# Kernel tuning notes

Measured on AMD Instinct MI355X. Metric: run time of the kernel, lower is better.

The kernel has to match this reference:

```python
import jax, jax.numpy as jnp
import numpy as np

N = 50000   # nodes
E = 1600000 # edges
G = 256     # graphs
EPS = 1e-5  # batchnorm eps (torch default)


def _bn(h, g, b):
    # training-mode BatchNorm1d: biased batch stats
    m = h.mean(0)
    v = h.var(0)
    return (h - m) * jax.lax.rsqrt(v + EPS) * g + b


def _mlp(h, W1, b1, g, be, W2, b2):
    # Lin -> BN -> ReLU -> Lin
    h = jax.nn.relu(_bn(h @ W1 + b1, g, be))
    return h @ W2 + b2


def _scatter_mean(v, idx, n):
    s = jax.ops.segment_sum(v, idx, num_segments=n)
    c = jax.ops.segment_sum(jnp.ones((v.shape[0], 1), v.dtype), idx, num_segments=n)
    return s / jnp.maximum(c, 1.0)


def setup_inputs() -> dict:
    key = jax.random.key(0)
    ks = iter(jax.random.split(key, 32))
    d = {}
    d["x"] = jax.random.normal(next(ks), (N, 48), dtype=jnp.float32)
    d["edge_index"] = jax.random.randint(next(ks), (2, E), 0, N, dtype=jnp.int64)
    d["batch"] = jnp.sort(jax.random.randint(next(ks), (N,), 0, G, dtype=jnp.int64))

    def lin(k, fin, fout):
        kw, kb = jax.random.split(k)
        s = 1.0 / np.sqrt(fin)
        return (jax.random.uniform(kw, (fin, fout), jnp.float32, -s, s),
                jax.random.uniform(kb, (fout,), jnp.float32, -s, s))

    # input BatchNorm1d(48)
    d["bn_g"] = jnp.ones((48,), jnp.float32)
    d["bn_b"] = jnp.zeros((48,), jnp.float32)

    def mlp_params(prefix, fin, fmid, fout):
        W1, b1 = lin(next(ks), fin, fmid)
        W2, b2 = lin(next(ks), fmid, fout)
        d[prefix + "_W1"], d[prefix + "_b1"] = W1, b1
        d[prefix + "_g"] = jnp.ones((fmid,), jnp.float32)
        d[prefix + "_be"] = jnp.zeros((fmid,), jnp.float32)
        d[prefix + "_W2"], d[prefix + "_b2"] = W2, b2

    mlp_params("e", 96, 128, 128)    # EdgeBlock
    mlp_params("n1", 176, 128, 128)  # NodeBlock mlp1
    mlp_params("n2", 176, 128, 128)  # NodeBlock mlp2
    mlp_params("gl", 128, 128, 2)    # GlobalBlock
    return d


def reference(x, edge_index, batch, bn_g, bn_b,
              e_W1, e_b1, e_g, e_be, e_W2, e_b2,
              n1_W1, n1_b1, n1_g, n1_be, n1_W2, n1_b2,
              n2_W1, n2_b1, n2_g, n2_be, n2_W2, n2_b2,
              gl_W1, gl_b1, gl_g, gl_be, gl_W2, gl_b2):
    x = _bn(x, bn_g, bn_b)
    row, col = edge_index[0], edge_index[1]
    # EdgeBlock: cat(src, dest) -> MLP
    edge_attr = _mlp(jnp.concatenate([x[row], x[col]], axis=1),
                     e_W1, e_b1, e_g, e_be, e_W2, e_b2)
    # NodeBlock: cat(x[row], edge_attr) -> mlp1 -> scatter_mean(col) -> cat(x,.) -> mlp2
    m = _mlp(jnp.concatenate([x[row], edge_attr], axis=1),
             n1_W1, n1_b1, n1_g, n1_be, n1_W2, n1_b2)
    agg = _scatter_mean(m, col, N)
    x2 = _mlp(jnp.concatenate([x, agg], axis=1),
              n2_W1, n2_b1, n2_g, n2_be, n2_W2, n2_b2)
    # GlobalBlock: scatter_mean over graphs -> MLP -> [G, 2]
    u = _scatter_mean(x2, batch, G)
    u = _mlp(u, gl_W1, gl_b1, gl_g, gl_be, gl_W2, gl_b2)
    return u
```

## Files before the change

### kernel.cpp

```cpp
#include <hip/hip_runtime.h>
#include <hip/hip_bf16.h>
#include <stdint.h>

#define DEV static __device__ __forceinline__

constexpr int N_ = 50000;
constexpr int E_ = 1600000;
constexpr int G_ = 256;

typedef __attribute__((ext_vector_type(8))) short short8;
typedef __attribute__((ext_vector_type(4))) float float4v;

DEV uint16_t f2bf(float f){
  uint32_t u = __float_as_uint(f);
  uint32_t r = (u + 0x7fffu + ((u >> 16) & 1u)) >> 16;
  return (uint16_t)r;
}
DEV float bf2f(uint16_t v){ return __uint_as_float((uint32_t)v << 16); }
DEV void unpack2(uint32_t p, float& a, float& b){
  a = __uint_as_float(p << 16);
  b = __uint_as_float(p & 0xffff0000u);
}
DEV uint32_t pack2(float a, float b){
  return (uint32_t)f2bf(a) | ((uint32_t)f2bf(b) << 16);
}
DEV short8 lds_load8(const uint16_t* p){
  union { short8 v; uint2 u[2]; } c;
  c.u[0] = *(const uint2*)p;
  c.u[1] = *(const uint2*)(p + 4);
  return c.v;
}
DEV void lds_store16B_as8(uint32_t* d, uint4 v){
  *(uint2*)d       = make_uint2(v.x, v.y);
  *(uint2*)(d + 2) = make_uint2(v.z, v.w);
}

__global__ __launch_bounds__(256) void k_xstats(const float* __restrict__ x, float* __restrict__ xstats){
  __shared__ float lst[96];
  int t = threadIdx.x;
  if (t < 96) lst[t] = 0.f;
  __syncthreads();
  int gid = blockIdx.x * 256 + t;
  int c4 = (gid % 12) * 4;
  float s[4] = {0,0,0,0}, q[4] = {0,0,0,0};
  const float4v* x4 = (const float4v*)x;
  for (int i = gid; i < N_ * 12; i += 64512){
    float4v v = x4[i];
    #pragma unroll
    for (int j = 0; j < 4; j++){ s[j] += v[j]; q[j] += v[j]*v[j]; }
  }
  #pragma unroll
  for (int j = 0; j < 4; j++){
    atomicAdd(&lst[c4 + j], s[j]);
    atomicAdd(&lst[48 + c4 + j], q[j]);
  }
  __syncthreads();
  if (t < 96) atomicAdd(&xstats[t], lst[t]);
}

__global__ void k_xfin(const float* __restrict__ xstats, const float* __restrict__ g,
                       const float* __restrict__ b, float* __restrict__ sx, float* __restrict__ tx){
  int c = threadIdx.x;
  if (c < 48){
    float m = xstats[c] / (float)N_;
    float v = xstats[48 + c] / (float)N_ - m*m;
    float s = g[c] / sqrtf(v + 1e-5f);
    sx[c] = s; tx[c] = b[c] - m*s;
  }
}

__global__ __launch_bounds__(256) void k_hist(const int* __restrict__ ei, int* __restrict__ counts){
  int e = blockIdx.x * 256 + threadIdx.x;
  if (e < E_) atomicAdd(&counts[ei[E_ + e]], 1);
}

__global__ __launch_bounds__(256) void k_invc(const int* __restrict__ counts, float* __restrict__ invc){
  int n = blockIdx.x * 256 + threadIdx.x;
  if (n < N_){ int c = counts[n]; invc[n] = (c > 0) ? 1.f/(float)c : 0.f; }
}

__global__ __launch_bounds__(256) void k_scan(const int* __restrict__ counts, int* __restrict__ off, int* __restrict__ cur){
  __shared__ int wsum[4];
  __shared__ int carry_s;
  int t = threadIdx.x, lane = t & 63, w = t >> 6;
  if (t == 0) carry_s = 0;
  __syncthreads();
  for (int base = 0; base < N_; base += 1024){
    int i0 = base + t * 4;
    int v0 = (i0 + 0 < N_) ? counts[i0 + 0] : 0;
    int v1 = (i0 + 1 < N_) ? counts[i0 + 1] : 0;
    int v2 = (i0 + 2 < N_) ? counts[i0 + 2] : 0;
    int v3 = (i0 + 3 < N_) ? counts[i0 + 3] : 0;
    int tsum = v0 + v1 + v2 + v3;
    int xs = tsum;
    for (int d = 1; d < 64; d <<= 1){ int y = __shfl_up(xs, d); if (lane >= d) xs += y; }
    if (lane == 63) wsum[w] = xs;
    __syncthreads();
    int woff = 0;
    for (int k = 0; k < w; k++) woff += wsum[k];
    int excl = xs - tsum + woff + carry_s;
    int e0 = excl, e1 = e0 + v0, e2 = e1 + v1, e3 = e2 + v2;
    if (i0 + 0 < N_){ off[i0+0] = e0; cur[i0+0] = e0; }
    if (i0 + 1 < N_){ off[i0+1] = e1; cur[i0+1] = e1; }
    if (i0 + 2 < N_){ off[i0+2] = e2; cur[i0+2] = e2; }
    if (i0 + 3 < N_){ off[i0+3] = e3; cur[i0+3] = e3; }
    __syncthreads();
    if (t == 0) carry_s += wsum[0] + wsum[1] + wsum[2] + wsum[3];
    __syncthreads();
  }
  if (t == 0) off[N_] = carry_s;
}

__global__ __launch_bounds__(256) void k_place(const int* __restrict__ ei, int* __restrict__ cur,
                                               int2* __restrict__ rcs){
  int e = blockIdx.x * 256 + threadIdx.x;
  if (e < E_){
    int c = ei[E_ + e];
    int p = atomicAdd(&cur[c], 1);
    rcs[p] = make_int2(ei[e], c);
  }
}

__global__ __launch_bounds__(256) void k_wprep(
    const float* __restrict__ eW2, const float* __restrict__ n1W1,
    const float* __restrict__ n1W2, const float* __restrict__ n2W1,
    const float* __restrict__ n2W2, const float* __restrict__ glW1,
    const float* __restrict__ n1b2, const float* __restrict__ n2b2,
    uint16_t* __restrict__ Mt, float* __restrict__ Wcomb,
    float* __restrict__ M3, float* __restrict__ c1, float* __restrict__ c3){
  int flat = blockIdx.x * 256 + threadIdx.x;
  if (flat < 16384){
    int n = flat & 127, k = flat >> 7;
    float a = 0.f;
    for (int j = 0; j < 128; j++) a += eW2[k*128 + j] * n1W1[(48 + j)*128 + n];
    Mt[n*128 + k] = f2bf(a);
  } else if (flat < 32768){
    int b = flat - 16384;
    int n = b & 127, j = b >> 7;
    float a = 0.f;
    for (int m = 0; m < 128; m++) a += n1W2[j*128 + m] * n2W1[(48 + m)*128 + n];
    Wcomb[(48 + j)*128 + n] = a;
  } else if (flat < 38912){
    int b = flat - 32768;
    int n = b & 127, k = b >> 7;
    Wcomb[k*128 + n] = n2W1[k*128 + n];
  } else if (flat < 55296){
    int b = flat - 38912;
    int n = b & 127, j = b >> 7;
    float a = 0.f;
    for (int m = 0; m < 128; m++) a += n2W2[j*128 + m] * glW1[m*128 + n];
    M3[j*128 + n] = a;
  } else if (flat < 55552){
    int e = flat - 55296;
    if (e < 128){
      float a = 0.f;
      for (int m = 0; m < 128; m++) a += n1b2[m] * n2W1[(48 + m)*128 + e];
      c1[e] = a;
    } else {
      int n = e - 128;
      float a = 0.f;
      for (int m = 0; m < 128; m++) a += n2b2[m] * glW1[m*128 + n];
      c3[n] = a;
    }
  }
}

__global__ __launch_bounds__(256) void k_nodegemm(
    const float* __restrict__ x, const float* __restrict__ sx, const float* __restrict__ tx,
    const float* __restrict__ eW1, const float* __restrict__ n1W1,
    uint16_t* __restrict__ AC, uint16_t* __restrict__ Bn){
  __shared__ float xT[48][36];
  __shared__ float W[48][128];
  int t = threadIdx.x;
  int n0 = blockIdx.x * 32;
  for (int idx = t; idx < 384; idx += 256){
    int r = idx / 12, q = idx % 12;
    int n = n0 + r;
    float4v v = {0.f,0.f,0.f,0.f};
    if (n < N_) v = *(const float4v*)&x[(size_t)n*48 + q*4];
    #pragma unroll
    for (int i = 0; i < 4; i++){
      int k = q*4 + i;
      xT[k][r] = v[i] * sx[k] + tx[k];
    }
  }
  int cg = t & 31, ng = t >> 5;
  const float* Wsrc0 = eW1;
  const float* Wsrc1 = eW1 + 48*128;
  const float* Wsrc2 = n1W1;
  for (int seg = 0; seg < 3; seg++){
    const float* Wsrc = (seg == 0) ? Wsrc0 : (seg == 1) ? Wsrc1 : Wsrc2;
    __syncthreads();
    {
      const float4v* src4 = (const float4v*)Wsrc;
      float4v* W4 = (float4v*)W;
      for (int idx = t; idx < 1536; idx += 256) W4[idx] = src4[idx];
    }
    __syncthreads();
    float acc[4][4] = {{0.f}};
    #pragma unroll 4
    for (int k = 0; k < 48; k++){
      float4v xv = *(const float4v*)&xT[k][ng*4];
      float4v wv = *(const float4v*)&W[k][cg*4];
      #pragma unroll
      for (int i = 0; i < 4; i++)
        #pragma unroll
        for (int j = 0; j < 4; j++)
          acc[i][j] += xv[i]*wv[j];
    }
    #pragma unroll
    for (int i = 0; i < 4; i++){
      int n = n0 + ng*4 + i;
      if (n >= N_) continue;
      uint2 pv;
      pv.x = pack2(acc[i][0], acc[i][1]);
      pv.y = pack2(acc[i][2], acc[i][3]);
      if (seg == 0)      *(uint2*)&AC[(size_t)n*256 + cg*4] = pv;
      else if (seg == 1) *(uint2*)&Bn[(size_t)n*128 + cg*4] = pv;
      else               *(uint2*)&AC[(size_t)n*256 + 128 + cg*4] = pv;
    }
  }
}

__global__ __launch_bounds__(256) void k_estats(const int2* __restrict__ rcs,
    const uint16_t* __restrict__ AC, const uint16_t* __restrict__ Bn, float* __restrict__ estR){
  __shared__ float red[4][64][4];
  __shared__ float lst[256];
  int t = threadIdx.x, lane = t & 63, w = t >> 6;
  int wid = blockIdx.x * 4 + w, nw = gridDim.x * 4;
  float s0=0,q0=0,s1=0,q1=0;
  const uint32_t* ACu = (const uint32_t*)AC;
  const uint32_t* Bu  = (const uint32_t*)Bn;
  for (int e = wid; e < E_; e += nw){
    int2 rc = rcs[e];
    uint32_t pa = ACu[(size_t)rc.x*128 + lane];
    uint32_t pb = Bu[(size_t)rc.y*64 + lane];
    float a0,a1,b0,b1; unpack2(pa,a0,a1); unpack2(pb,b0,b1);
    float h0 = a0 + b0, h1 = a1 + b1;
    s0 += h0; q0 += h0*h0; s1 += h1; q1 += h1*h1;
  }
  red[w][lane][0]=s0; red[w][lane][1]=q0; red[w][lane][2]=s1; red[w][lane][3]=q1;
  __syncthreads();
  if (t < 64){
    float S0=0,Q0=0,S1=0,Q1=0;
    for (int ww = 0; ww < 4; ww++){ S0+=red[ww][t][0]; Q0+=red[ww][t][1]; S1+=red[ww][t][2]; Q1+=red[ww][t][3]; }
    lst[2*t] = S0; lst[2*t+1] = S1; lst[128+2*t] = Q0; lst[128+2*t+1] = Q1;
  }
  __syncthreads();
  atomicAdd(&estR[(blockIdx.x & 63)*256 + t], lst[t]);
}

__global__ void k_bnfin(const float* __restrict__ statsR, int reps, const float* __restrict__ g,
                        const float* __restrict__ be, float* __restrict__ s_out, float* __restrict__ t_out,
                        float inv_n){
  int c = threadIdx.x;
  if (c >= 128) return;
  float sm = 0.f, sq = 0.f;
  for (int r = 0; r < reps; r++){ sm += statsR[r*256 + c]; sq += statsR[r*256 + 128 + c]; }
  float m = sm * inv_n;
  float v = sq * inv_n - m*m;
  float s = g[c] / sqrtf(v + 1e-5f);
  s_out[c] = s;
  t_out[c] = be[c] - m*s;
}


__global__ __launch_bounds__(256) void k_epass0(
    const int2* __restrict__ rcs,
    const uint16_t* __restrict__ AC, const uint16_t* __restrict__ Bn,
    const uint16_t* __restrict__ Mt, const float* __restrict__ se, const float* __restrict__ te,
    float* __restrict__ n1R){
  __shared__ __align__(16) uint16_t bufA[64*132];
  __shared__ __align__(16) uint16_t bufB[128*132];
  __shared__ __align__(16) float sete[256];
  __shared__ float lst[256];
  __shared__ int srow[64], scol[64];
  const int t = threadIdx.x;
  const long i0 = (long)blockIdx.x * 64;
  const int lane = t & 63, w = t >> 6;
  const int m = lane & 15, quad = lane >> 4;

  if (t < 128){ sete[t] = se[t]; sete[128 + t] = te[t]; }
  lst[t] = 0.f;
  if (t < 64){ int2 rc = rcs[i0 + t]; srow[t] = rc.x; scol[t] = rc.y; }
  __syncthreads();

  {
    int e = t >> 2, q = t & 3;
    int r = srow[e], c = scol[e];
    const uint4* Ap = (const uint4*)((const uint32_t*)AC + (size_t)r*128 + q*16);
    const uint4* Bp = (const uint4*)((const uint32_t*)Bn + (size_t)c*64  + q*16);
    uint32_t* dstd = (uint32_t*)bufA + e*66 + q*16;
    int cb = q*32;
    #pragma unroll
    for (int u = 0; u < 4; u++){
      uint4 va = Ap[u], vb = Bp[u];
      float4v sA = *(const float4v*)&sete[cb + u*8];
      float4v sB = *(const float4v*)&sete[cb + u*8 + 4];
      float4v tA = *(const float4v*)&sete[128 + cb + u*8];
      float4v tB = *(const float4v*)&sete[128 + cb + u*8 + 4];
      float a0,a1,b0,b1; uint4 o;
      unpack2(va.x,a0,a1); unpack2(vb.x,b0,b1);
      o.x = pack2(fmaxf(0.f,(a0+b0)*sA[0]+tA[0]), fmaxf(0.f,(a1+b1)*sA[1]+tA[1]));
      unpack2(va.y,a0,a1); unpack2(vb.y,b0,b1);
      o.y = pack2(fmaxf(0.f,(a0+b0)*sA[2]+tA[2]), fmaxf(0.f,(a1+b1)*sA[3]+tA[3]));
      unpack2(va.z,a0,a1); unpack2(vb.z,b0,b1);
      o.z = pack2(fmaxf(0.f,(a0+b0)*sB[0]+tB[0]), fmaxf(0.f,(a1+b1)*sB[1]+tB[1]));
      unpack2(va.w,a0,a1); unpack2(vb.w,b0,b1);
      o.w = pack2(fmaxf(0.f,(a0+b0)*sB[2]+tB[2]), fmaxf(0.f,(a1+b1)*sB[3]+tB[3]));
      lds_store16B_as8(dstd + u*4, o);
    }
  }
  {
    int n = t >> 1, h = t & 1;
    const uint4* src = (const uint4*)((const uint32_t*)Mt + n*64 + h*32);
    uint32_t* dstd = (uint32_t*)bufB + n*66 + h*32;
    #pragma unroll
    for (int u = 0; u < 8; u++) lds_store16B_as8(dstd + u*4, src[u]);
  }
  __syncthreads();

  float4v acc[8];
  #pragma unroll
  for (int nt = 0; nt < 8; nt++){ acc[nt][0]=0.f; acc[nt][1]=0.f; acc[nt][2]=0.f; acc[nt][3]=0.f; }
  {
    const uint16_t* aptr = bufA + (w*16 + m)*132 + quad*8;
    const uint16_t* bbase = bufB + m*132 + quad*8;
    #pragma unroll
    for (int ks = 0; ks < 4; ks++){
      short8 af = lds_load8(aptr + ks*32);
      #pragma unroll
      for (int nt = 0; nt < 8; nt++){
        short8 bf = lds_load8(bbase + nt*16*132 + ks*32);
        acc[nt] = __builtin_amdgcn_mfma_f32_16x16x32_bf16(af, bf, acc[nt], 0, 0, 0);
      }
    }
  }
  __syncthreads();

  {
    int e = t >> 2, q = t & 3;
    int r = srow[e];
    const uint4* src = (const uint4*)((const uint32_t*)AC + (size_t)r*128 + 64 + q*16);
    uint32_t* dstd = (uint32_t*)bufA + e*66 + q*16;
    #pragma unroll
    for (int u = 0; u < 4; u++) lds_store16B_as8(dstd + u*4, src[u]);
  }
  #pragma unroll
  for (int nt = 0; nt < 8; nt++)
    #pragma unroll
    for (int reg = 0; reg < 4; reg++)
      bufB[(w*16 + quad*4 + reg)*132 + nt*16 + m] = f2bf(acc[nt][reg]);
  __syncthreads();

  {
    int cp = t & 63, eg = t >> 6;
    float ss0=0,qq0=0,ss1=0,qq1=0;
    #pragma unroll
    for (int it = 0; it < 16; it++){
      int e = it*4 + eg;
      uint32_t ph = ((uint32_t*)bufB)[e*66 + cp];
      uint32_t pc = ((uint32_t*)bufA)[e*66 + cp];
      float h0,h1,c0,c1v;
      unpack2(ph,h0,h1); unpack2(pc,c0,c1v);
      float v0 = h0 + c0, v1 = h1 + c1v;
      ss0 += v0; qq0 += v0*v0; ss1 += v1; qq1 += v1*v1;
    }
    atomicAdd(&lst[2*cp], ss0);
    atomicAdd(&lst[2*cp+1], ss1);
    atomicAdd(&lst[128+2*cp], qq0);
    atomicAdd(&lst[128+2*cp+1], qq1);
  }
  __syncthreads();
  atomicAdd(&n1R[(blockIdx.x & 63)*256 + t], lst[t]);
}

__global__ __launch_bounds__(256) void k_epass1(
    const int2* __restrict__ rcs,
    const uint16_t* __restrict__ AC, const uint16_t* __restrict__ Bn,
    const uint16_t* __restrict__ Mt, const float* __restrict__ se, const float* __restrict__ te,
    const float* __restrict__ sn1, const float* __restrict__ tn1,
    float* __restrict__ aggf){
  __shared__ __align__(16) uint16_t bufA[64*132];
  __shared__ __align__(16) uint16_t bufB[128*132];
  __shared__ __align__(16) float sete[256];
  __shared__ int srow[64], scol[64];
  __shared__ int snseg;
  const int t = threadIdx.x;
  const long i0 = (long)blockIdx.x * 64;
  const int lane = t & 63, w = t >> 6;
  const int m = lane & 15, quad = lane >> 4;

  uint32_t* bufBu = (uint32_t*)bufB;
  float* segacc  = (float*)(bufBu + 4224);
  float* sn1c    = (float*)(bufBu + 7296);
  float* tn1c    = (float*)(bufBu + 7424);
  int*   ssid_s  = (int*)(bufBu + 7552);
  int*   scseg_s = (int*)(bufBu + 7616);

  if (t < 128){ sete[t] = se[t]; sete[128 + t] = te[t]; }
  if (t < 64){ int2 rc = rcs[i0 + t]; srow[t] = rc.x; scol[t] = rc.y; }
  __syncthreads();

  {
    int e = t >> 2, q = t & 3;
    int r = srow[e], c = scol[e];
    const uint4* Ap = (const uint4*)((const uint32_t*)AC + (size_t)r*128 + q*16);
    const uint4* Bp = (const uint4*)((const uint32_t*)Bn + (size_t)c*64  + q*16);
    uint32_t* dstd = (uint32_t*)bufA + e*66 + q*16;
    int cb = q*32;
    #pragma unroll
    for (int u = 0; u < 4; u++){
      uint4 va = Ap[u], vb = Bp[u];
      float4v sA = *(const float4v*)&sete[cb + u*8];
      float4v sB = *(const float4v*)&sete[cb + u*8 + 4];
      float4v tA = *(const float4v*)&sete[128 + cb + u*8];
      float4v tB = *(const float4v*)&sete[128 + cb + u*8 + 4];
      float a0,a1,b0,b1; uint4 o;
      unpack2(va.x,a0,a1); unpack2(vb.x,b0,b1);
      o.x = pack2(fmaxf(0.f,(a0+b0)*sA[0]+tA[0]), fmaxf(0.f,(a1+b1)*sA[1]+tA[1]));
      unpack2(va.y,a0,a1); unpack2(vb.y,b0,b1);
      o.y = pack2(fmaxf(0.f,(a0+b0)*sA[2]+tA[2]), fmaxf(0.f,(a1+b1)*sA[3]+tA[3]));
      unpack2(va.z,a0,a1); unpack2(vb.z,b0,b1);
      o.z = pack2(fmaxf(0.f,(a0+b0)*sB[0]+tB[0]), fmaxf(0.f,(a1+b1)*sB[1]+tB[1]));
      unpack2(va.w,a0,a1); unpack2(vb.w,b0,b1);
      o.w = pack2(fmaxf(0.f,(a0+b0)*sB[2]+tB[2]), fmaxf(0.f,(a1+b1)*sB[3]+tB[3]));
      lds_store16B_as8(dstd + u*4, o);
    }
  }
  {
    int n = t >> 1, h = t & 1;
    const uint4* src = (const uint4*)((const uint32_t*)Mt + n*64 + h*32);
    uint32_t* dstd = bufBu + n*66 + h*32;
    #pragma unroll
    for (int u = 0; u < 8; u++) lds_store16B_as8(dstd + u*4, src[u]);
  }
  __syncthreads();

  float4v acc[8];
  #pragma unroll
  for (int nt = 0; nt < 8; nt++){ acc[nt][0]=0.f; acc[nt][1]=0.f; acc[nt][2]=0.f; acc[nt][3]=0.f; }
  {
    const uint16_t* aptr = bufA + (w*16 + m)*132 + quad*8;
    const uint16_t* bbase = bufB + m*132 + quad*8;
    #pragma unroll
    for (int ks = 0; ks < 4; ks++){
      short8 af = lds_load8(aptr + ks*32);
      #pragma unroll
      for (int nt = 0; nt < 8; nt++){
        short8 bf = lds_load8(bbase + nt*16*132 + ks*32);
        acc[nt] = __builtin_amdgcn_mfma_f32_16x16x32_bf16(af, bf, acc[nt], 0, 0, 0);
      }
    }
  }
  __syncthreads();

  {
    int e = t >> 2, q = t & 3;
    int r = srow[e];
    const uint4* src = (const uint4*)((const uint32_t*)AC + (size_t)r*128 + 64 + q*16);
    uint32_t* dstd = (uint32_t*)bufA + e*66 + q*16;
    #pragma unroll
    for (int u = 0; u < 4; u++) lds_store16B_as8(dstd + u*4, src[u]);
  }
  #pragma unroll
  for (int nt = 0; nt < 8; nt++)
    #pragma unroll
    for (int reg = 0; reg < 4; reg++)
      bufB[(w*16 + quad*4 + reg)*132 + nt*16 + m] = f2bf(acc[nt][reg]);
  if (t < 64){
    bool bnd = (t > 0) && (scol[t] != scol[t-1]);
    unsigned long long mask = __ballot(bnd);
    int sid = __popcll(mask << (63 - t));
    ssid_s[t] = sid;
    if (bnd || t == 0) scseg_s[sid] = scol[t];
    if (t == 63) snseg = sid + 1;
  } else if (t < 192){
    int c = t - 64;
    sn1c[c] = sn1[c]; tn1c[c] = tn1[c];
  }
  for (int i = t; i < 24*128; i += 256) segacc[i] = 0.f;
  __syncthreads();

  {
    int cp = t & 63, eg = t >> 6;
    float s0 = sn1c[2*cp], s1 = sn1c[2*cp+1];
    float b0 = tn1c[2*cp], b1 = tn1c[2*cp+1];
    int nseg = snseg;
    bool lp = (nseg <= 24);
    int cursid = ssid_s[eg*16];
    float r0 = 0.f, r1 = 0.f;
    for (int it = 0; it < 16; it++){
      int e = eg*16 + it;
      uint32_t ph = bufBu[e*66 + cp];
      uint32_t pc = ((uint32_t*)bufA)[e*66 + cp];
      float h0,h1,c0,c1v;
      unpack2(ph,h0,h1); unpack2(pc,c0,c1v);
      float v0 = fmaxf(0.f, (h0+c0)*s0 + b0);
      float v1 = fmaxf(0.f, (h1+c1v)*s1 + b1);
      int sid = ssid_s[e];
      if (sid != cursid){
        if (lp){ atomicAdd(&segacc[cursid*128 + 2*cp], r0); atomicAdd(&segacc[cursid*128 + 2*cp+1], r1); }
        else { int c = scseg_s[cursid];
               atomicAdd(&aggf[(size_t)c*128 + 2*cp], r0); atomicAdd(&aggf[(size_t)c*128 + 2*cp+1], r1); }
        cursid = sid; r0 = 0.f; r1 = 0.f;
      }
      r0 += v0; r1 += v1;
    }
    if (lp){ atomicAdd(&segacc[cursid*128 + 2*cp], r0); atomicAdd(&segacc[cursid*128 + 2*cp+1], r1); }
    else { int c = scseg_s[cursid];
           atomicAdd(&aggf[(size_t)c*128 + 2*cp], r0); atomicAdd(&aggf[(size_t)c*128 + 2*cp+1], r1); }
    __syncthreads();
    if (lp){
      for (int idx = t; idx < nseg*64; idx += 256){
        int s = idx >> 6, cpp = idx & 63;
        float v0 = segacc[s*128 + 2*cpp], v1 = segacc[s*128 + 2*cpp+1];
        int c = scseg_s[s];
        float* dst = &aggf[(size_t)c*128 + 2*cpp];
        if (s == 0 || s == nseg - 1){ atomicAdd(dst, v0); atomicAdd(dst+1, v1); }
        else { dst[0] = v0; dst[1] = v1; }
      }
    }
  }
}

__global__ __launch_bounds__(256) void k_n2(const float* __restrict__ x,
    const float* __restrict__ sx, const float* __restrict__ tx,
    const float* __restrict__ aggf, const float* __restrict__ invc,
    const float* __restrict__ Wc, const float* __restrict__ c1, const int* __restrict__ counts,
    float* __restrict__ hn2, float* __restrict__ n2R){
  __shared__ float xT[44][36];
  __shared__ float wT[44][128];
  __shared__ float lst[256];
  int t = threadIdx.x;
  int n0 = blockIdx.x * 32;
  int cg = t & 31, ng = t >> 5;
  lst[t] = 0.f;
  float acc[4][4] = {{0.f}};
  for (int kc = 0; kc < 176; kc += 44){
    __syncthreads();
    for (int idx = t; idx < 32*44; idx += 256){
      int r = idx / 44, k = idx % 44;
      int n = n0 + r, kk = kc + k;
      float v = 0.f;
      if (n < N_){
        if (kk < 48) v = x[(size_t)n*48 + kk] * sx[kk] + tx[kk];
        else         v = aggf[(size_t)n*128 + (kk - 48)] * invc[n];
      }
      xT[k][r] = v;
    }
    for (int idx = t; idx < 44*128; idx += 256){
      int k = idx >> 7, c = idx & 127;
      wT[k][c] = Wc[(kc + k)*128 + c];
    }
    __syncthreads();
    for (int k = 0; k < 44; k++){
      float4v xv = *(const float4v*)&xT[k][ng*4];
      float4v wv = *(const float4v*)&wT[k][cg*4];
      #pragma unroll
      for (int i = 0; i < 4; i++)
        #pragma unroll
        for (int j = 0; j < 4; j++)
          acc[i][j] += xv[i]*wv[j];
    }
  }
  float csum[4] = {0,0,0,0}, cqs[4] = {0,0,0,0};
  for (int i = 0; i < 4; i++){
    int n = n0 + ng*4 + i;
    if (n >= N_) continue;
    bool ok = counts[n] > 0;
    float4v o;
    #pragma unroll
    for (int j = 0; j < 4; j++){
      float vv = acc[i][j] + (ok ? c1[cg*4 + j] : 0.f);
      o[j] = vv; csum[j] += vv; cqs[j] += vv*vv;
    }
    *(float4v*)&hn2[(size_t)n*128 + cg*4] = o;
  }
  #pragma unroll
  for (int j = 0; j < 4; j++){
    atomicAdd(&lst[cg*4 + j], csum[j]);
    atomicAdd(&lst[128 + cg*4 + j], cqs[j]);
  }
  __syncthreads();
  atomicAdd(&n2R[(blockIdx.x & 63)*256 + t], lst[t]);
}

__global__ void k_goff(const int* __restrict__ batch, int* __restrict__ goff){
  int g = threadIdx.x;
  int lo = 0, hi = N_;
  while (lo < hi){ int mid = (lo + hi) >> 1; if (batch[mid] < g) lo = mid + 1; else hi = mid; }
  goff[g] = lo;
  if (g == 0) goff[256] = N_;
}

__global__ __launch_bounds__(128) void k_gmean(const float* __restrict__ hn2, const int* __restrict__ goff,
    const float* __restrict__ sn2, const float* __restrict__ tn2, float* __restrict__ gmean){
  int g = blockIdx.x, c = threadIdx.x;
  int b = goff[g], e = goff[g+1];
  float s = sn2[c], tt = tn2[c], a = 0.f;
  for (int r = b; r < e; r++) a += fmaxf(0.f, hn2[(size_t)r*128 + c]*s + tt);
  gmean[g*128 + c] = (e > b) ? a/(float)(e - b) : 0.f;
}

__global__ __launch_bounds__(256) void k_hg(const float* __restrict__ gmean, const float* __restrict__ M3,
    const float* __restrict__ c3, const int* __restrict__ goff,
    float* __restrict__ hg, float* __restrict__ gls){
  int idx = blockIdx.x * 256 + threadIdx.x;
  int g = idx >> 7, c = idx & 127;
  float a = 0.f;
  for (int k = 0; k < 128; k++) a += gmean[g*128 + k] * M3[k*128 + c];
  if (goff[g+1] > goff[g]) a += c3[c];
  hg[idx] = a;
  atomicAdd(&gls[c], a);
  atomicAdd(&gls[128 + c], a*a);
}

__global__ __launch_bounds__(256) void k_out(const float* __restrict__ hg, const float* __restrict__ sgl,
    const float* __restrict__ tgl, const float* __restrict__ glW2, const float* __restrict__ glb2,
    float* __restrict__ out){
  int idx = blockIdx.x * 256 + threadIdx.x;
  int g = idx >> 1, o = idx & 1;
  float a = 0.f;
  for (int c = 0; c < 128; c++){
    float r = fmaxf(0.f, hg[g*128 + c]*sgl[c] + tgl[c]);
    a += r * glW2[c*2 + o];
  }
  out[idx] = a + glb2[o];
}

extern "C" void kernel_launch(void* const* d_in, const int* in_sizes, int n_in,
                              void* d_out, int out_size, void* d_ws, size_t ws_size,
                              hipStream_t stream){
  const float* x     = (const float*)d_in[0];
  const int*   ei    = (const int*)d_in[1];
  const int*   batch = (const int*)d_in[2];
  const float* bn_g  = (const float*)d_in[3];
  const float* bn_b  = (const float*)d_in[4];
  const float* eW1   = (const float*)d_in[5];
  const float* e_g   = (const float*)d_in[7];
  const float* e_be  = (const float*)d_in[8];
  const float* eW2   = (const float*)d_in[9];
  const float* n1W1  = (const float*)d_in[11];
  const float* n1_g  = (const float*)d_in[13];
  const float* n1_be = (const float*)d_in[14];
  const float* n1W2  = (const float*)d_in[15];
  const float* n1b2  = (const float*)d_in[16];
  const float* n2W1  = (const float*)d_in[17];
  const float* n2_g  = (const float*)d_in[19];
  const float* n2_be = (const float*)d_in[20];
  const float* n2W2  = (const float*)d_in[21];
  const float* n2b2  = (const float*)d_in[22];
  const float* glW1  = (const float*)d_in[23];
  const float* gl_g  = (const float*)d_in[25];
  const float* gl_be = (const float*)d_in[26];
  const float* glW2  = (const float*)d_in[27];
  const float* glb2  = (const float*)d_in[28];
  float* out = (float*)d_out;

  char* w = (char*)d_ws;
  size_t off = 0;
  auto take = [&](size_t bytes) -> char* {
    char* p = w + off;
    off = (off + bytes + 511) & ~(size_t)511;
    return p;
  };

  const size_t ZONE_WORDS = 96 + 3*64*256 + 256 + N_;
  float* zone   = (float*)take(ZONE_WORDS * 4);
  float* xstats = zone;
  float* estR   = zone + 96;
  float* n1R    = zone + 96 + 64*256;
  float* n2R    = zone + 96 + 2*64*256;
  float* gls    = zone + 96 + 3*64*256;
  int*   counts = (int*)(zone + 96 + 3*64*256 + 256);

  float* sx = (float*)take(48*4);   float* tx = (float*)take(48*4);
  float* se = (float*)take(128*4);  float* te = (float*)take(128*4);
  float* sn1 = (float*)take(128*4); float* tn1 = (float*)take(128*4);
  float* sn2 = (float*)take(128*4); float* tn2 = (float*)take(128*4);
  float* sgl = (float*)take(128*4); float* tgl = (float*)take(128*4);
  float* c1 = (float*)take(128*4);  float* c3 = (float*)take(128*4);
  float* invc  = (float*)take((size_t)N_*4);
  float* Wcomb = (float*)take(176*128*4);
  float* M3    = (float*)take(128*128*4);
  float* gmean = (float*)take(G_*128*4);
  float* hg    = (float*)take(G_*128*4);
  int* offs = (int*)take((N_+1)*4);
  int* cur  = (int*)take(N_*4);
  int* goff = (int*)take(257*4);
  uint16_t* Mt = (uint16_t*)take(128*128*2);
  uint16_t* AC = (uint16_t*)take((size_t)N_*256*2);
  uint16_t* Bn = (uint16_t*)take((size_t)N_*128*2);
  float* aggf  = (float*)take((size_t)N_*128*4);
  float* hn2   = (float*)take((size_t)N_*128*4);
  int2* rcs = (int2*)take((size_t)E_*8);

  if (off > ws_size) return;

  hipMemsetAsync(zone, 0, ZONE_WORDS*4, stream);
  hipMemsetAsync(aggf, 0, (size_t)N_*128*4, stream);

  hipLaunchKernelGGL(k_xstats, dim3(252), dim3(256), 0, stream, x, xstats);
  hipLaunchKernelGGL(k_hist, dim3((E_+255)/256), dim3(256), 0, stream, ei, counts);
  hipLaunchKernelGGL(k_xfin, dim3(1), dim3(64), 0, stream, xstats, bn_g, bn_b, sx, tx);
  hipLaunchKernelGGL(k_scan, dim3(1), dim3(256), 0, stream, counts, offs, cur);
  hipLaunchKernelGGL(k_place, dim3((E_+255)/256), dim3(256), 0, stream, ei, cur, rcs);
  hipLaunchKernelGGL(k_invc, dim3((N_+255)/256), dim3(256), 0, stream, counts, invc);
  hipLaunchKernelGGL(k_wprep, dim3(217), dim3(256), 0, stream,
                     eW2, n1W1, n1W2, n2W1, n2W2, glW1, n1b2, n2b2, Mt, Wcomb, M3, c1, c3);
  hipLaunchKernelGGL(k_nodegemm, dim3((N_+31)/32), dim3(256), 0, stream,
                     x, sx, tx, eW1, n1W1, AC, Bn);
  hipLaunchKernelGGL(k_estats, dim3(1024), dim3(256), 0, stream, rcs, AC, Bn, estR);
  hipLaunchKernelGGL(k_bnfin, dim3(1), dim3(128), 0, stream, estR, 64, e_g, e_be, se, te, 1.f/(float)E_);
  hipLaunchKernelGGL(k_epass0, dim3(E_/64), dim3(256), 0, stream,
                     rcs, AC, Bn, Mt, se, te, n1R);
  hipLaunchKernelGGL(k_bnfin, dim3(1), dim3(128), 0, stream, n1R, 64, n1_g, n1_be, sn1, tn1, 1.f/(float)E_);
  hipLaunchKernelGGL(k_epass1, dim3(E_/64), dim3(256), 0, stream,
                     rcs, AC, Bn, Mt, se, te, sn1, tn1, aggf);
  hipLaunchKernelGGL(k_n2, dim3((N_+31)/32), dim3(256), 0, stream,
                     x, sx, tx, aggf, invc, Wcomb, c1, counts, hn2, n2R);
  hipLaunchKernelGGL(k_bnfin, dim3(1), dim3(128), 0, stream, n2R, 64, n2_g, n2_be, sn2, tn2, 1.f/(float)N_);
  hipLaunchKernelGGL(k_goff, dim3(1), dim3(256), 0, stream, batch, goff);
  hipLaunchKernelGGL(k_gmean, dim3(256), dim3(128), 0, stream, hn2, goff, sn2, tn2, gmean);
  hipLaunchKernelGGL(k_hg, dim3(128), dim3(256), 0, stream, gmean, M3, c3, goff, hg, gls);
  hipLaunchKernelGGL(k_bnfin, dim3(1), dim3(128), 0, stream, gls, 1, gl_g, gl_be, sgl, tgl, 1.f/(float)G_);
  hipLaunchKernelGGL(k_out, dim3(2), dim3(256), 0, stream, hg, sgl, tgl, glW2, glb2, out);
}
```

Before: 1.552 ms.

## Parallelize CSR scan into three kernels and prefetch edge gathers into registers

```diff
diff --git a/kernel.cpp b/kernel.cpp
--- a/kernel.cpp
+++ b/kernel.cpp
@@ -79,36 +79,47 @@
   if (n < N_){ int c = counts[n]; invc[n] = (c > 0) ? 1.f/(float)c : 0.f; }
 }
 
-__global__ __launch_bounds__(256) void k_scan(const int* __restrict__ counts, int* __restrict__ off, int* __restrict__ cur){
-  __shared__ int wsum[4];
-  __shared__ int carry_s;
-  int t = threadIdx.x, lane = t & 63, w = t >> 6;
-  if (t == 0) carry_s = 0;
-  __syncthreads();
-  for (int base = 0; base < N_; base += 1024){
-    int i0 = base + t * 4;
-    int v0 = (i0 + 0 < N_) ? counts[i0 + 0] : 0;
-    int v1 = (i0 + 1 < N_) ? counts[i0 + 1] : 0;
-    int v2 = (i0 + 2 < N_) ? counts[i0 + 2] : 0;
-    int v3 = (i0 + 3 < N_) ? counts[i0 + 3] : 0;
-    int tsum = v0 + v1 + v2 + v3;
-    int xs = tsum;
-    for (int d = 1; d < 64; d <<= 1){ int y = __shfl_up(xs, d); if (lane >= d) xs += y; }
-    if (lane == 63) wsum[w] = xs;
-    __syncthreads();
-    int woff = 0;
-    for (int k = 0; k < w; k++) woff += wsum[k];
-    int excl = xs - tsum + woff + carry_s;
-    int e0 = excl, e1 = e0 + v0, e2 = e1 + v1, e3 = e2 + v2;
-    if (i0 + 0 < N_){ off[i0+0] = e0; cur[i0+0] = e0; }
-    if (i0 + 1 < N_){ off[i0+1] = e1; cur[i0+1] = e1; }
-    if (i0 + 2 < N_){ off[i0+2] = e2; cur[i0+2] = e2; }
-    if (i0 + 3 < N_){ off[i0+3] = e3; cur[i0+3] = e3; }
-    __syncthreads();
-    if (t == 0) carry_s += wsum[0] + wsum[1] + wsum[2] + wsum[3];
-    __syncthreads();
-  }
-  if (t == 0) off[N_] = carry_s;
+__global__ __launch_bounds__(256) void k_scanA(const int* __restrict__ counts, int* __restrict__ bsum){
+  __shared__ int ws[4];
+  int b = blockIdx.x, t = threadIdx.x, lane = t & 63, w = t >> 6;
+  int i0 = b*1024 + t*4;
+  int s = 0;
+  #pragma unroll
+  for (int j = 0; j < 4; j++){ int i = i0 + j; if (i < N_) s += counts[i]; }
+  for (int d = 1; d < 64; d <<= 1) s += __shfl_xor(s, d);
+  if (lane == 0) ws[w] = s;
+  __syncthreads();
+  if (t == 0) bsum[b] = ws[0] + ws[1] + ws[2] + ws[3];
+}
+__global__ void k_scanB(const int* __restrict__ bsum, int* __restrict__ boff, int* __restrict__ off, int nb){
+  int t = threadIdx.x;
+  int v = (t < nb) ? bsum[t] : 0;
+  int x = v;
+  for (int d = 1; d < 64; d <<= 1){ int y = __shfl_up(x, d); if (t >= d) x += y; }
+  if (t < nb) boff[t] = x - v;
+  if (t == 63) off[N_] = x;
+}
+__global__ __launch_bounds__(256) void k_scanC(const int* __restrict__ counts, const int* __restrict__ boff,
+                                               int* __restrict__ off, int* __restrict__ cur){
+  __shared__ int ws[4];
+  int b = blockIdx.x, t = threadIdx.x, lane = t & 63, w = t >> 6;
+  int i0 = b*1024 + t*4;
+  int v0 = (i0+0 < N_) ? counts[i0+0] : 0;
+  int v1 = (i0+1 < N_) ? counts[i0+1] : 0;
+  int v2 = (i0+2 < N_) ? counts[i0+2] : 0;
+  int v3 = (i0+3 < N_) ? counts[i0+3] : 0;
+  int ts = v0+v1+v2+v3, xs = ts;
+  for (int d = 1; d < 64; d <<= 1){ int y = __shfl_up(xs, d); if (lane >= d) xs += y; }
+  if (lane == 63) ws[w] = xs;
+  __syncthreads();
+  int woff = 0;
+  for (int k = 0; k < w; k++) woff += ws[k];
+  int excl = xs - ts + woff + boff[b];
+  int e0 = excl, e1 = e0+v0, e2 = e1+v1, e3 = e2+v2;
+  if (i0+0 < N_){ off[i0+0] = e0; cur[i0+0] = e0; }
+  if (i0+1 < N_){ off[i0+1] = e1; cur[i0+1] = e1; }
+  if (i0+2 < N_){ off[i0+2] = e2; cur[i0+2] = e2; }
+  if (i0+3 < N_){ off[i0+3] = e3; cur[i0+3] = e3; }
 }
 
 __global__ __launch_bounds__(256) void k_place(const int* __restrict__ ei, int* __restrict__ cur,
@@ -274,27 +285,32 @@
   __shared__ __align__(16) uint16_t bufB[128*132];
   __shared__ __align__(16) float sete[256];
   __shared__ float lst[256];
-  __shared__ int srow[64], scol[64];
   const int t = threadIdx.x;
   const long i0 = (long)blockIdx.x * 64;
   const int lane = t & 63, w = t >> 6;
   const int m = lane & 15, quad = lane >> 4;
+  const int e = t >> 2, q = t & 3;
+
+  int2 rc = rcs[i0 + e];
+  const uint4* Ap = (const uint4*)((const uint32_t*)AC + (size_t)rc.x*128 + q*16);
+  const uint4* Bp = (const uint4*)((const uint32_t*)Bn + (size_t)rc.y*64  + q*16);
+  const uint4* Cp = (const uint4*)((const uint32_t*)AC + (size_t)rc.x*128 + 64 + q*16);
+  uint4 va0 = Ap[0], va1 = Ap[1], va2 = Ap[2], va3 = Ap[3];
+  uint4 vb0 = Bp[0], vb1 = Bp[1], vb2 = Bp[2], vb3 = Bp[3];
+  uint4 vc0 = Cp[0], vc1 = Cp[1], vc2 = Cp[2], vc3 = Cp[3];
 
   if (t < 128){ sete[t] = se[t]; sete[128 + t] = te[t]; }
   lst[t] = 0.f;
-  if (t < 64){ int2 rc = rcs[i0 + t]; srow[t] = rc.x; scol[t] = rc.y; }
-  __syncthreads();
-
-  {
-    int e = t >> 2, q = t & 3;
-    int r = srow[e], c = scol[e];
-    const uint4* Ap = (const uint4*)((const uint32_t*)AC + (size_t)r*128 + q*16);
-    const uint4* Bp = (const uint4*)((const uint32_t*)Bn + (size_t)c*64  + q*16);
+  __syncthreads();
+
+  {
     uint32_t* dstd = (uint32_t*)bufA + e*66 + q*16;
     int cb = q*32;
+    uint4 vas[4] = {va0, va1, va2, va3};
+    uint4 vbs[4] = {vb0, vb1, vb2, vb3};
     #pragma unroll
     for (int u = 0; u < 4; u++){
-      uint4 va = Ap[u], vb = Bp[u];
+      uint4 va = vas[u], vb = vbs[u];
       float4v sA = *(const float4v*)&sete[cb + u*8];
       float4v sB = *(const float4v*)&sete[cb + u*8 + 4];
       float4v tA = *(const float4v*)&sete[128 + cb + u*8];
@@ -339,12 +355,11 @@
   __syncthreads();
 
   {
-    int e = t >> 2, q = t & 3;
-    int r = srow[e];
-    const uint4* src = (const uint4*)((const uint32_t*)AC + (size_t)r*128 + 64 + q*16);
     uint32_t* dstd = (uint32_t*)bufA + e*66 + q*16;
-    #pragma unroll
-    for (int u = 0; u < 4; u++) lds_store16B_as8(dstd + u*4, src[u]);
+    lds_store16B_as8(dstd + 0,  vc0);
+    lds_store16B_as8(dstd + 4,  vc1);
+    lds_store16B_as8(dstd + 8,  vc2);
+    lds_store16B_as8(dstd + 12, vc3);
   }
   #pragma unroll
   for (int nt = 0; nt < 8; nt++)
@@ -358,9 +373,9 @@
     float ss0=0,qq0=0,ss1=0,qq1=0;
     #pragma unroll
     for (int it = 0; it < 16; it++){
-      int e = it*4 + eg;
-      uint32_t ph = ((uint32_t*)bufB)[e*66 + cp];
-      uint32_t pc = ((uint32_t*)bufA)[e*66 + cp];
+      int ee = it*4 + eg;
+      uint32_t ph = ((uint32_t*)bufB)[ee*66 + cp];
+      uint32_t pc = ((uint32_t*)bufA)[ee*66 + cp];
       float h0,h1,c0,c1v;
       unpack2(ph,h0,h1); unpack2(pc,c0,c1v);
       float v0 = h0 + c0, v1 = h1 + c1v;
@@ -384,34 +399,46 @@
   __shared__ __align__(16) uint16_t bufA[64*132];
   __shared__ __align__(16) uint16_t bufB[128*132];
   __shared__ __align__(16) float sete[256];
-  __shared__ int srow[64], scol[64];
+  __shared__ int ssid_s[64], scseg_s[64];
   __shared__ int snseg;
   const int t = threadIdx.x;
   const long i0 = (long)blockIdx.x * 64;
   const int lane = t & 63, w = t >> 6;
   const int m = lane & 15, quad = lane >> 4;
+  const int e = t >> 2, q = t & 3;
 
   uint32_t* bufBu = (uint32_t*)bufB;
-  float* segacc  = (float*)(bufBu + 4224);
-  float* sn1c    = (float*)(bufBu + 7296);
-  float* tn1c    = (float*)(bufBu + 7424);
-  int*   ssid_s  = (int*)(bufBu + 7552);
-  int*   scseg_s = (int*)(bufBu + 7616);
+  float* segacc = (float*)(bufBu + 4224);
+
+  int2 rc = rcs[i0 + e];
+  const uint4* Ap = (const uint4*)((const uint32_t*)AC + (size_t)rc.x*128 + q*16);
+  const uint4* Bp = (const uint4*)((const uint32_t*)Bn + (size_t)rc.y*64  + q*16);
+  const uint4* Cp = (const uint4*)((const uint32_t*)AC + (size_t)rc.x*128 + 64 + q*16);
+  uint4 va0 = Ap[0], va1 = Ap[1], va2 = Ap[2], va3 = Ap[3];
+  uint4 vb0 = Bp[0], vb1 = Bp[1], vb2 = Bp[2], vb3 = Bp[3];
+  uint4 vc0 = Cp[0], vc1 = Cp[1], vc2 = Cp[2], vc3 = Cp[3];
 
   if (t < 128){ sete[t] = se[t]; sete[128 + t] = te[t]; }
-  if (t < 64){ int2 rc = rcs[i0 + t]; srow[t] = rc.x; scol[t] = rc.y; }
-  __syncthreads();
-
-  {
-    int e = t >> 2, q = t & 3;
-    int r = srow[e], c = scol[e];
-    const uint4* Ap = (const uint4*)((const uint32_t*)AC + (size_t)r*128 + q*16);
-    const uint4* Bp = (const uint4*)((const uint32_t*)Bn + (size_t)c*64  + q*16);
+  if (t < 64){
+    int myc = rcs[i0 + t].y;
+    int prevc = (t > 0) ? rcs[i0 + t - 1].y : myc;
+    bool bnd = (t > 0) && (myc != prevc);
+    unsigned long long mask = __ballot(bnd);
+    int sid = __popcll(mask << (63 - t));
+    ssid_s[t] = sid;
+    if (bnd || t == 0) scseg_s[sid] = myc;
+    if (t == 63) snseg = sid + 1;
+  }
+  __syncthreads();
+
+  {
     uint32_t* dstd = (uint32_t*)bufA + e*66 + q*16;
     int cb = q*32;
+    uint4 vas[4] = {va0, va1, va2, va3};
+    uint4 vbs[4] = {vb0, vb1, vb2, vb3};
     #pragma unroll
     for (int u = 0; u < 4; u++){
-      uint4 va = Ap[u], vb = Bp[u];
+      uint4 va = vas[u], vb = vbs[u];
       float4v sA = *(const float4v*)&sete[cb + u*8];
       float4v sB = *(const float4v*)&sete[cb + u*8 + 4];
       float4v tA = *(const float4v*)&sete[128 + cb + u*8];
@@ -456,49 +483,38 @@
   __syncthreads();
 
   {
-    int e = t >> 2, q = t & 3;
-    int r = srow[e];
-    const uint4* src = (const uint4*)((const uint32_t*)AC + (size_t)r*128 + 64 + q*16);
     uint32_t* dstd = (uint32_t*)bufA + e*66 + q*16;
-    #pragma unroll
-    for (int u = 0; u < 4; u++) lds_store16B_as8(dstd + u*4, src[u]);
+    lds_store16B_as8(dstd + 0,  vc0);
+    lds_store16B_as8(dstd + 4,  vc1);
+    lds_store16B_as8(dstd + 8,  vc2);
+    lds_store16B_as8(dstd + 12, vc3);
   }
   #pragma unroll
   for (int nt = 0; nt < 8; nt++)
     #pragma unroll
     for (int reg = 0; reg < 4; reg++)
       bufB[(w*16 + quad*4 + reg)*132 + nt*16 + m] = f2bf(acc[nt][reg]);
-  if (t < 64){
-    bool bnd = (t > 0) && (scol[t] != scol[t-1]);
-    unsigned long long mask = __ballot(bnd);
-    int sid = __popcll(mask << (63 - t));
-    ssid_s[t] = sid;
-    if (bnd || t == 0) scseg_s[sid] = scol[t];
-    if (t == 63) snseg = sid + 1;
-  } else if (t < 192){
-    int c = t - 64;
-    sn1c[c] = sn1[c]; tn1c[c] = tn1[c];
-  }
+  if (t < 128){ sete[t] = sn1[t]; sete[128 + t] = tn1[t]; }
   for (int i = t; i < 24*128; i += 256) segacc[i] = 0.f;
   __syncthreads();
 
   {
     int cp = t & 63, eg = t >> 6;
-    float s0 = sn1c[2*cp], s1 = sn1c[2*cp+1];
-    float b0 = tn1c[2*cp], b1 = tn1c[2*cp+1];
+    float s0 = sete[2*cp], s1 = sete[2*cp+1];
+    float b0 = sete[128+2*cp], b1 = sete[128+2*cp+1];
     int nseg = snseg;
     bool lp = (nseg <= 24);
     int cursid = ssid_s[eg*16];
     float r0 = 0.f, r1 = 0.f;
     for (int it = 0; it < 16; it++){
-      int e = eg*16 + it;
-      uint32_t ph = bufBu[e*66 + cp];
-      uint32_t pc = ((uint32_t*)bufA)[e*66 + cp];
+      int ee = eg*16 + it;
+      uint32_t ph = bufBu[ee*66 + cp];
+      uint32_t pc = ((uint32_t*)bufA)[ee*66 + cp];
       float h0,h1,c0,c1v;
       unpack2(ph,h0,h1); unpack2(pc,c0,c1v);
       float v0 = fmaxf(0.f, (h0+c0)*s0 + b0);
       float v1 = fmaxf(0.f, (h1+c1v)*s1 + b1);
-      int sid = ssid_s[e];
+      int sid = ssid_s[ee];
       if (sid != cursid){
         if (lp){ atomicAdd(&segacc[cursid*128 + 2*cp], r0); atomicAdd(&segacc[cursid*128 + 2*cp+1], r1); }
         else { int c = scseg_s[cursid];
@@ -689,6 +705,8 @@
   int* offs = (int*)take((N_+1)*4);
   int* cur  = (int*)take(N_*4);
   int* goff = (int*)take(257*4);
+  int* bsum = (int*)take(64*4);
+  int* boff = (int*)take(64*4);
   uint16_t* Mt = (uint16_t*)take(128*128*2);
   uint16_t* AC = (uint16_t*)take((size_t)N_*256*2);
   uint16_t* Bn = (uint16_t*)take((size_t)N_*128*2);
@@ -701,10 +719,13 @@
   hipMemsetAsync(zone, 0, ZONE_WORDS*4, stream);
   hipMemsetAsync(aggf, 0, (size_t)N_*128*4, stream);
 
+  const int NB = (N_ + 1023) / 1024;
   hipLaunchKernelGGL(k_xstats, dim3(252), dim3(256), 0, stream, x, xstats);
   hipLaunchKernelGGL(k_hist, dim3((E_+255)/256), dim3(256), 0, stream, ei, counts);
   hipLaunchKernelGGL(k_xfin, dim3(1), dim3(64), 0, stream, xstats, bn_g, bn_b, sx, tx);
-  hipLaunchKernelGGL(k_scan, dim3(1), dim3(256), 0, stream, counts, offs, cur);
+  hipLaunchKernelGGL(k_scanA, dim3(NB), dim3(256), 0, stream, counts, bsum);
+  hipLaunchKernelGGL(k_scanB, dim3(1), dim3(64), 0, stream, bsum, boff, offs, NB);
+  hipLaunchKernelGGL(k_scanC, dim3(NB), dim3(256), 0, stream, counts, boff, offs, cur);
   hipLaunchKernelGGL(k_place, dim3((E_+255)/256), dim3(256), 0, stream, ei, cur, rcs);
   hipLaunchKernelGGL(k_invc, dim3((N_+255)/256), dim3(256), 0, stream, counts, invc);
   hipLaunchKernelGGL(k_wprep, dim3(217), dim3(256), 0, stream,
```

Result: no change. 1.524 ms (-1.8%).
